# Kernel optimization log

Measured on AMD Instinct MI355X. Metric: run time of the kernel, lower is better.

The kernel has to match this reference:

```python
import jax, jax.numpy as jnp
import numpy as np

HEADS, FOLD_W, FOLD_H, PW, PH = 4, 2, 2, 2, 2


def setup_inputs() -> dict:
    key = jax.random.key(0)
    ks = jax.random.split(key, 4)
    B, C, W0, H0 = 64, 128, 56, 56
    hd = HEADS * 24  # 96
    return {
        "x": jax.random.normal(ks[0], (B, C, W0, H0), jnp.float32),
        "Wc": jax.random.normal(ks[1], (hd, C), jnp.float32) * 0.05,
        "bc": jnp.zeros((hd,), jnp.float32),
        "Wp": jax.random.normal(ks[2], (hd, C), jnp.float32) * 0.05,
        "bp": jnp.zeros((hd,), jnp.float32),
        "sim_alpha": jnp.ones((1,), jnp.float32),
        "sim_beta": jnp.zeros((1,), jnp.float32),
        "Wo": jax.random.normal(ks[3], (C, hd), jnp.float32) * 0.05,
        "bo": jnp.zeros((C,), jnp.float32),
    }


def _conv1x1(t, W, b):
    return jnp.einsum('oc,bcwh->bowh', W, t) + b[None, :, None, None]


def _forward(x, Wc, bc, Wp, bp, sim_alpha, sim_beta, Wo, bo):
    B, C, W0, H0 = x.shape
    value = _conv1x1(x, Wp, bp)   # [B, e*c, W0, H0]
    q = _conv1x1(x, Wc, bc)
    hd = q.shape[1] // HEADS
    # 'b (e c) w h -> (b e) c w h'
    split = lambda t: t.reshape(B * HEADS, hd, W0, H0)
    value, q = split(value), split(q)
    # fold: 'b c (f1 w) (f2 h) -> (b f1 f2) c w h'
    w2, h2 = W0 // FOLD_W, H0 // FOLD_H
    def fold(t):
        b0 = t.shape[0]
        return (t.reshape(b0, hd, FOLD_W, w2, FOLD_H, h2)
                 .transpose(0, 2, 4, 1, 3, 5)
                 .reshape(b0 * FOLD_W * FOLD_H, hd, w2, h2))
    value, q = fold(value), fold(q)
    b, c, w, h = q.shape
    # adaptive avg pool to (PW, PH): mean over equal blocks
    def adpool(t):
        return t.reshape(b, c, PW, w // PW, PH, h // PH).mean(axis=(3, 5))
    centers = adpool(q).reshape(b, c, PW * PH).transpose(0, 2, 1)          # [b, M, c]
    value_centers = adpool(value).reshape(b, c, PW * PH).transpose(0, 2, 1)
    qf = q.reshape(b, c, w * h).transpose(0, 2, 1)                          # [b, N, c]
    vf = value.reshape(b, c, w * h).transpose(0, 2, 1)
    eps = 1e-12
    cn = centers / jnp.clip(jnp.linalg.norm(centers, axis=-1, keepdims=True), eps)
    xn = qf / jnp.clip(jnp.linalg.norm(qf, axis=-1, keepdims=True), eps)
    sim = jax.nn.sigmoid(sim_beta + sim_alpha * jnp.einsum('bmc,bnc->bmn', cn, xn))  # [b, M, N]
    # hard top-1 assignment over centers axis
    idx = jnp.argmax(sim, axis=1)                                           # [b, N]
    mask = (jnp.arange(sim.shape[1])[None, :, None] == idx[:, None, :])
    sim = sim * mask
    # weighted combine (segment-sum over patches) instead of huge broadcast
    cluster = (jnp.einsum('bmn,bnc->bmc', sim, vf) + value_centers) / (sim.sum(-1, keepdims=True) + 1.0)
    patches = jnp.einsum('bmn,bmc->bnc', sim, cluster)                      # [b, N, c]
    patches = patches.transpose(0, 2, 1).reshape(b, c, w, h)
    # unfold: '(b f1 f2) c w h -> b c (f1 w) (f2 h)'
    patches = (patches.reshape(B * HEADS, FOLD_W, FOLD_H, c, w, h)
                      .transpose(0, 3, 1, 4, 2, 5)
                      .reshape(B * HEADS, c, W0, H0))
    patches = patches.reshape(B, HEADS * c, W0, H0)
    return _conv1x1(patches, Wo, bo)


def reference(x, Wc, bc, Wp, bp, sim_alpha, sim_beta, Wo, bo):
    return _forward(x, Wc, bc, Wp, bp, sim_alpha, sim_beta, Wo, bo)
```

## Files before the change

kernel.cpp:

```cpp
#include <hip/hip_runtime.h>
#include <math.h>

#define CIN 128
#define HD  96
#define SP  3136
#define ROW 56
#define SLAB 1568
#define YSTRIDE 9216

__global__ __launch_bounds__(256) void wtq_k(
    const float* __restrict__ Wc, float* __restrict__ Wt)
{
  const int idx = blockIdx.x * 256 + threadIdx.x;
  if (idx >= 96 * 128) return;
  const int o = idx >> 7, c = idx & 127;
  Wt[c * 96 + o] = Wc[idx];
}

__global__ __launch_bounds__(256) void pe_k(
    const float* __restrict__ Wo, const float* __restrict__ Wp,
    const float* __restrict__ bp, float* __restrict__ P, float* __restrict__ obp)
{
  const int e = blockIdx.x;
  __shared__ float ws[24][128];
  const int tid = threadIdx.x;
  for (int i = tid; i < 24 * 128; i += 256)
    ws[i >> 7][i & 127] = Wp[(size_t)(e * 24 + (i >> 7)) * CIN + (i & 127)];
  __syncthreads();
  const int co = tid & 127;
  const int cig = tid >> 7;
  float wo_r[24];
  #pragma unroll
  for (int c = 0; c < 24; ++c) wo_r[c] = Wo[(size_t)co * HD + e * 24 + c];
  for (int ci = cig * 64; ci < cig * 64 + 64; ++ci) {
    float s = 0.f;
    #pragma unroll
    for (int c = 0; c < 24; ++c) s = fmaf(wo_r[c], ws[c][ci], s);
    P[((size_t)e * 128 + ci) * 128 + co] = s;
  }
  if (cig == 0) {
    float s = 0.f;
    #pragma unroll
    for (int c = 0; c < 24; ++c) s = fmaf(wo_r[c], bp[e * 24 + c], s);
    obp[e * 128 + co] = s;
  }
}

__global__ __launch_bounds__(128) void q_conv(
    const float* __restrict__ x, const float* __restrict__ Wt,
    const float* __restrict__ bc, float* __restrict__ qbuf)
{
  const int st = blockIdx.x % 49;
  const int b  = blockIdx.x / 49;
  const float* xb = x + (size_t)b * CIN * SP + st * 64;

  __shared__ float xs[32][64];
  __shared__ float wl[32][96];

  const int tid = threadIdx.x;
  const int og = tid >> 4;
  const int sg = tid & 15;

  float acc[12][4];
  #pragma unroll
  for (int i = 0; i < 12; ++i) { acc[i][0]=0.f; acc[i][1]=0.f; acc[i][2]=0.f; acc[i][3]=0.f; }

  for (int kt = 0; kt < 4; ++kt) {
    __syncthreads();
    #pragma unroll
    for (int r = 0; r < 4; ++r) {
      const int i = tid + r * 128;
      const int cc = i >> 4, s4 = i & 15;
      float4 v = *reinterpret_cast<const float4*>(xb + (size_t)(kt*32 + cc) * SP + s4*4);
      *reinterpret_cast<float4*>(&xs[cc][s4*4]) = v;
    }
    #pragma unroll
    for (int r = 0; r < 6; ++r) {
      const int i = tid + r * 128;
      const int cl = i / 24, o4 = i % 24;
      float4 wv = *reinterpret_cast<const float4*>(Wt + (size_t)(kt*32 + cl) * 96 + o4*4);
      *reinterpret_cast<float4*>(&wl[cl][o4*4]) = wv;
    }
    __syncthreads();
    #pragma unroll
    for (int cc = 0; cc < 32; ++cc) {
      float xv[4];
      *reinterpret_cast<float4*>(xv) = *reinterpret_cast<const float4*>(&xs[cc][sg*4]);
      float wv[12];
      *reinterpret_cast<float4*>(wv + 0) = *reinterpret_cast<const float4*>(&wl[cc][og*12 + 0]);
      *reinterpret_cast<float4*>(wv + 4) = *reinterpret_cast<const float4*>(&wl[cc][og*12 + 4]);
      *reinterpret_cast<float4*>(wv + 8) = *reinterpret_cast<const float4*>(&wl[cc][og*12 + 8]);
      #pragma unroll
      for (int i = 0; i < 12; ++i)
        #pragma unroll
        for (int j = 0; j < 4; ++j)
          acc[i][j] = fmaf(wv[i], xv[j], acc[i][j]);
    }
  }
  #pragma unroll
  for (int i = 0; i < 12; ++i) {
    const int o = og * 12 + i;
    const float bias = bc[o];
    float4 v;
    v.x = acc[i][0] + bias; v.y = acc[i][1] + bias;
    v.z = acc[i][2] + bias; v.w = acc[i][3] + bias;
    *reinterpret_cast<float4*>(qbuf + ((size_t)b*96 + o) * SP + st*64 + sg*4) = v;
  }
}

__global__ __launch_bounds__(512, 4) void cluster_k(
    float* qbuf, const float* __restrict__ alpha_p, const float* __restrict__ beta_p)
{
  const int blk = blockIdx.x;
  const int f1  = blk & 1;
  const int be  = blk >> 1;
  const size_t base = (size_t)be * 24 * SP + (size_t)(f1 * 28) * ROW;
  float* qp = qbuf + base;

  __shared__ double cnd[24][8];
  __shared__ float  sbest[SLAB];
  __shared__ unsigned char ibest[SLAB];
  __shared__ float dnl[8];

  const int tid  = threadIdx.x;
  const int wid  = tid >> 6;
  const int lane = tid & 63;

  for (int c = wid; c < 24; c += 8) {
    const float* src = qp + (size_t)c * SP;
    double b0=0,b1=0,b2=0,b3=0,b4=0,b5=0,b6=0,b7=0;
    for (int n = lane; n < SLAB; n += 64) {
      const int w = n / 56, h = n - w * 56;
      const int hf = (h >= 28) ? (h - 28) : h;
      const int g  = ((h >= 28) ? 4 : 0) + ((w >= 14) ? 2 : 0) + ((hf >= 14) ? 1 : 0);
      const double val = (double)src[n];
      b0 += (g==0)?val:0.0; b1 += (g==1)?val:0.0;
      b2 += (g==2)?val:0.0; b3 += (g==3)?val:0.0;
      b4 += (g==4)?val:0.0; b5 += (g==5)?val:0.0;
      b6 += (g==6)?val:0.0; b7 += (g==7)?val:0.0;
    }
    #pragma unroll
    for (int m = 32; m >= 1; m >>= 1) {
      b0 += __shfl_xor(b0,m); b1 += __shfl_xor(b1,m);
      b2 += __shfl_xor(b2,m); b3 += __shfl_xor(b3,m);
      b4 += __shfl_xor(b4,m); b5 += __shfl_xor(b5,m);
      b6 += __shfl_xor(b6,m); b7 += __shfl_xor(b7,m);
    }
    if (lane == 0) {
      cnd[c][0]=b0*(1.0/196.0); cnd[c][1]=b1*(1.0/196.0);
      cnd[c][2]=b2*(1.0/196.0); cnd[c][3]=b3*(1.0/196.0);
      cnd[c][4]=b4*(1.0/196.0); cnd[c][5]=b5*(1.0/196.0);
      cnd[c][6]=b6*(1.0/196.0); cnd[c][7]=b7*(1.0/196.0);
    }
  }
  __syncthreads();
  if (tid < 8) {
    double s = 0.0;
    #pragma unroll
    for (int c = 0; c < 24; ++c) { double t = cnd[c][tid]; s += t * t; }
    const double inv = 1.0 / fmax(sqrt(s), 1e-12);
    #pragma unroll
    for (int c = 0; c < 24; ++c) cnd[c][tid] *= inv;
  }
  __syncthreads();

  const double alpha = (double)alpha_p[0];
  const double beta  = (double)beta_p[0];

  for (int n0 = tid; n0 < SLAB; n0 += 512) {
    const int h  = n0 % 56;
    const int gb = (h >= 28) ? 4 : 0;
    double z0=0,z1=0,z2=0,z3=0,nrm=0;
    for (int c = 0; c < 24; ++c) {
      const double qv = (double)qp[(size_t)c * SP + n0];
      z0 += cnd[c][gb+0]*qv; z1 += cnd[c][gb+1]*qv;
      z2 += cnd[c][gb+2]*qv; z3 += cnd[c][gb+3]*qv;
      nrm += qv*qv;
    }
    const double inv = 1.0 / fmax(sqrt(nrm), 1e-12);
    const double v0 = beta + alpha * (z0 * inv);
    const double v1 = beta + alpha * (z1 * inv);
    const double v2 = beta + alpha * (z2 * inv);
    const double v3 = beta + alpha * (z3 * inv);
    double zb = v0; int bi = 0;
    if (v1 > zb) { zb = v1; bi = 1; }
    if (v2 > zb) { zb = v2; bi = 2; }
    if (v3 > zb) { zb = v3; bi = 3; }
    sbest[n0] = (float)(1.0 / (1.0 + exp(-zb)));
    ibest[n0] = (unsigned char)(gb + bi);
  }
  __syncthreads();

  if (wid < 8) {
    float dn = 0.f;
    for (int ch = 0; ch < 25; ++ch) {
      const int n = ch * 64 + lane;
      const bool p = (n < SLAB) && (ibest[n] == (unsigned char)wid);
      dn += p ? sbest[n] : 0.f;
    }
    #pragma unroll
    for (int m = 32; m >= 1; m >>= 1) dn += __shfl_xor(dn, m);
    if (lane == 0) dnl[wid] = dn;
  }
  __syncthreads();

  for (int i = tid; i < SLAB; i += 512) {
    qp[i] = sbest[i];
    reinterpret_cast<unsigned int*>(qp + SP)[i] = (unsigned int)ibest[i];
  }
  if (tid < 8) qp[2 * (size_t)SP + tid] = dnl[tid];
}

__global__ __launch_bounds__(256, 2) void seg_k(
    float* qbuf, const float* __restrict__ x)
{
  const int bid = blockIdx.x;
  const int wh  = bid & 1;
  const int f2  = (bid >> 1) & 1;
  const int f1  = (bid >> 2) & 1;
  const int b   = bid >> 3;

  __shared__ float4 sq_l[392];
  __shared__ unsigned int gq_l[392];
  __shared__ float xT[56][130];
  __shared__ float ysum[16][128];
  __shared__ float xps[2][128];

  const int tid = threadIdx.x;
  const int c   = tid & 127;
  const int pg  = tid >> 7;

  for (int n = tid; n < 392; n += 256) {
    const int r = n / 28, hc = n - r * 28;
    const int n_slab = (wh * 14 + r) * 56 + f2 * 28 + hc;
    float4 s4; unsigned int gp = 0;
    #pragma unroll
    for (int e = 0; e < 4; ++e) {
      const float* qp = qbuf + (size_t)(b*4 + e) * 24 * SP + (size_t)(f1*28) * ROW;
      const float sv = qp[n_slab];
      const unsigned int gv = reinterpret_cast<const unsigned int*>(qp + SP)[n_slab];
      if (e==0) s4.x = sv; else if (e==1) s4.y = sv;
      else if (e==2) s4.z = sv; else s4.w = sv;
      gp |= (gv & 3u) << (2*e);
    }
    sq_l[n] = s4; gq_l[n] = gp;
  }

  float sa[16];
  #pragma unroll
  for (int i = 0; i < 16; ++i) sa[i] = 0.f;
  float xp0 = 0.f, xp1 = 0.f;

  const float* xb = x + (size_t)b * CIN * SP;
  const int rowbase = f1*28 + wh*14;

  for (int ch = 0; ch < 7; ++ch) {
    __syncthreads();
    #pragma unroll
    for (int k = 0; k < 7; ++k) {
      const int slot = tid + k * 256;
      const int c2 = slot / 14, p4 = slot - c2 * 14;
      const int rr = p4 / 7, col4 = p4 - rr * 7;
      const int w = rowbase + ch*2 + rr;
      const float4 v = *reinterpret_cast<const float4*>(
          xb + (size_t)c2 * SP + (size_t)w * ROW + f2*28 + col4*4);
      const int pxl = rr * 28 + col4 * 4;
      xT[pxl+0][c2] = v.x; xT[pxl+1][c2] = v.y;
      xT[pxl+2][c2] = v.z; xT[pxl+3][c2] = v.w;
    }
    __syncthreads();
    for (int i = 0; i < 28; ++i) {
      const int pxl = 2*i + pg;
      const int n   = ch*56 + pxl;
      const float4 s4 = sq_l[n];
      const int gp = __builtin_amdgcn_readfirstlane((int)gq_l[n]);
      const float xv = xT[pxl][c];
      {
        const int k = gp & 3;
        if      (k == 0) sa[0]  += s4.x * xv;
        else if (k == 1) sa[1]  += s4.x * xv;
        else if (k == 2) sa[2]  += s4.x * xv;
        else             sa[3]  += s4.x * xv;
      }
      {
        const int k = (gp >> 2) & 3;
        if      (k == 0) sa[4]  += s4.y * xv;
        else if (k == 1) sa[5]  += s4.y * xv;
        else if (k == 2) sa[6]  += s4.y * xv;
        else             sa[7]  += s4.y * xv;
      }
      {
        const int k = (gp >> 4) & 3;
        if      (k == 0) sa[8]  += s4.z * xv;
        else if (k == 1) sa[9]  += s4.z * xv;
        else if (k == 2) sa[10] += s4.z * xv;
        else             sa[11] += s4.z * xv;
      }
      {
        const int k = (gp >> 6) & 3;
        if      (k == 0) sa[12] += s4.w * xv;
        else if (k == 1) sa[13] += s4.w * xv;
        else if (k == 2) sa[14] += s4.w * xv;
        else             sa[15] += s4.w * xv;
      }
      const int hc = (pxl >= 28) ? (pxl - 28) : pxl;
      if (hc >= 14) xp1 += xv; else xp0 += xv;
    }
  }

  __syncthreads();
  if (pg == 0) {
    #pragma unroll
    for (int k = 0; k < 16; ++k) ysum[k][c] = sa[k];
    xps[0][c] = xp0; xps[1][c] = xp1;
  }
  __syncthreads();
  if (pg == 1) {
    #pragma unroll
    for (int k = 0; k < 16; ++k) ysum[k][c] += sa[k];
    xps[0][c] += xp0; xps[1][c] += xp1;
  }
  __syncthreads();

  float* ybase = qbuf + ((size_t)b*96 + 9) * SP + (size_t)f1 * YSTRIDE;
  for (int i = tid; i < 16*128; i += 256) {
    const int row = i >> 7, cc = i & 127;
    ybase[((wh*2 + f2)*16 + row)*128 + cc] = ysum[row][cc];
  }
  {
    const int hb = tid >> 7, cc = tid & 127;
    ybase[64*128 + (f2*4 + wh*2 + hb)*128 + cc] = xps[hb][cc];
  }
}

__global__ __launch_bounds__(256) void proj_k(
    float* qbuf, const float* __restrict__ P, const float* __restrict__ obp)
{
  const int bid = blockIdx.x;
  const int b = bid >> 1, f1 = bid & 1;
  __shared__ float ylds[32][128];
  __shared__ float invs[32];
  const int tid = threadIdx.x;

  if (tid < 32) {
    const int e = tid >> 3, g = tid & 7;
    const float* dnp = qbuf + ((size_t)(b*4 + e) * 24 + 2) * SP + (size_t)(f1*28) * ROW;
    invs[tid] = 1.f / (dnp[g] + 1.f);
  }
  __syncthreads();

  const float* yp = qbuf + ((size_t)b*96 + 9) * SP + (size_t)f1 * YSTRIDE;
  for (int i = tid; i < 32*128; i += 256) {
    const int eg = i >> 7, cc = i & 127;
    const int e = eg >> 3, g = eg & 7, ff2 = g >> 2, m = g & 3;
    const float v = yp[((0 + ff2)*16 + e*4 + m)*128 + cc]
                  + yp[((2 + ff2)*16 + e*4 + m)*128 + cc]
                  + yp[64*128 + g*128 + cc] * (1.f/196.f);
    ylds[eg][cc] = v * invs[eg];
  }
  __syncthreads();

  const int co = tid & 127;
  const int e0 = (tid >> 7) * 2;
  float a0[8], a1[8];
  const float o0 = obp[e0 * 128 + co], o1 = obp[(e0 + 1) * 128 + co];
  #pragma unroll
  for (int g = 0; g < 8; ++g) { a0[g] = o0; a1[g] = o1; }
  for (int ci = 0; ci < 128; ++ci) {
    const float p0 = P[((size_t)e0 * 128 + ci) * 128 + co];
    const float p1 = P[((size_t)(e0 + 1) * 128 + ci) * 128 + co];
    #pragma unroll
    for (int g = 0; g < 8; ++g) {
      a0[g] = fmaf(p0, ylds[e0 * 8 + g][ci], a0[g]);
      a1[g] = fmaf(p1, ylds[(e0 + 1) * 8 + g][ci], a1[g]);
    }
  }
  float* pout = qbuf + ((size_t)b * 96 + 3 + f1 * 3) * SP;
  #pragma unroll
  for (int g = 0; g < 8; ++g) {
    pout[(e0 * 8 + g) * 128 + co]       = a0[g];
    pout[((e0 + 1) * 8 + g) * 128 + co] = a1[g];
  }
}

__global__ __launch_bounds__(256) void out_k(
    const float* __restrict__ qbuf, const float* __restrict__ bo,
    float* __restrict__ out)
{
  const int bid = blockIdx.x;
  const int b   = bid / 28;
  const int rem = bid % 28;
  const int f1  = rem / 14;
  const int rp  = rem % 14;
  const int n0  = rp * 112;

  __shared__ float  proj_l[4096];
  __shared__ float4 s_l4[112];
  __shared__ unsigned int g_l[112];
  __shared__ float  out_l[56 * 132];

  const int tid = threadIdx.x;

  {
    const float4* pg = reinterpret_cast<const float4*>(
        qbuf + ((size_t)b * 96 + 3 + f1*3) * SP);
    float4* pl = reinterpret_cast<float4*>(proj_l);
    #pragma unroll
    for (int r = 0; r < 4; ++r) pl[tid + r * 256] = pg[tid + r * 256];
  }
  for (int i = tid; i < 112; i += 256) {
    float4 sv; unsigned int gp = 0;
    #pragma unroll
    for (int e = 0; e < 4; ++e) {
      const float* sp = qbuf + ((size_t)(b*4 + e) * 24) * SP + (size_t)(f1*28) * ROW;
      const float sval = sp[n0 + i];
      const unsigned int gv = reinterpret_cast<const unsigned int*>(sp + SP)[n0 + i];
      if (e == 0) sv.x = sval; else if (e == 1) sv.y = sval;
      else if (e == 2) sv.z = sval; else sv.w = sval;
      gp |= (gv & 7u) << (8 * e);
    }
    s_l4[i] = sv; g_l[i] = gp;
  }
  __syncthreads();

  const int cq  = tid & 31;
  const int sub = tid >> 5;
  const float4 bo4 = *reinterpret_cast<const float4*>(bo + cq * 4);
  const float4* pl4 = reinterpret_cast<const float4*>(proj_l);

  for (int chunk = 0; chunk < 2; ++chunk) {
    const int pbase = chunk * 56;
    #pragma unroll
    for (int i = 0; i < 7; ++i) {
      const int pxl = sub * 7 + i;
      const int px  = pbase + pxl;
      const float4 sv = s_l4[px];
      const unsigned int gp = g_l[px];
      float4 acc = bo4;
      {
        const float4 p = pl4[(0*8 + (gp        & 7u)) * 32 + cq];
        acc.x = fmaf(sv.x, p.x, acc.x); acc.y = fmaf(sv.x, p.y, acc.y);
        acc.z = fmaf(sv.x, p.z, acc.z); acc.w = fmaf(sv.x, p.w, acc.w);
      }
      {
        const float4 p = pl4[(1*8 + ((gp >> 8) & 7u)) * 32 + cq];
        acc.x = fmaf(sv.y, p.x, acc.x); acc.y = fmaf(sv.y, p.y, acc.y);
        acc.z = fmaf(sv.y, p.z, acc.z); acc.w = fmaf(sv.y, p.w, acc.w);
      }
      {
        const float4 p = pl4[(2*8 + ((gp >> 16) & 7u)) * 32 + cq];
        acc.x = fmaf(sv.z, p.x, acc.x); acc.y = fmaf(sv.z, p.y, acc.y);
        acc.z = fmaf(sv.z, p.z, acc.z); acc.w = fmaf(sv.z, p.w, acc.w);
      }
      {
        const float4 p = pl4[(3*8 + ((gp >> 24) & 7u)) * 32 + cq];
        acc.x = fmaf(sv.w, p.x, acc.x); acc.y = fmaf(sv.w, p.y, acc.y);
        acc.z = fmaf(sv.w, p.z, acc.z); acc.w = fmaf(sv.w, p.w, acc.w);
      }
      *reinterpret_cast<float4*>(&out_l[pxl * 132 + cq * 4]) = acc;
    }
    __syncthreads();
    for (int t = tid; t < 128 * 56; t += 256) {
      const int co = t / 56, pxl = t - co * 56;
      out[((size_t)b * 128 + co) * SP + (size_t)f1 * SLAB + n0 + pbase + pxl] =
          out_l[pxl * 132 + co];
    }
    __syncthreads();
  }
}

extern "C" void kernel_launch(void* const* d_in, const int* in_sizes, int n_in,
                              void* d_out, int out_size, void* d_ws, size_t ws_size,
                              hipStream_t stream) {
  const float* x  = (const float*)d_in[0];
  const float* Wc = (const float*)d_in[1];
  const float* bc = (const float*)d_in[2];
  const float* Wp = (const float*)d_in[3];
  const float* bp = (const float*)d_in[4];
  const float* sa = (const float*)d_in[5];
  const float* sb = (const float*)d_in[6];
  const float* Wo = (const float*)d_in[7];
  const float* bo = (const float*)d_in[8];
  float* out  = (float*)d_out;
  float* qbuf = (float*)d_ws;
  float* Pbuf = out;
  float* obpb = out + 65536;
  float* Wtq  = out + 66048;

  wtq_k    <<<dim3(48),      dim3(256), 0, stream>>>(Wc, Wtq);
  pe_k     <<<dim3(4),       dim3(256), 0, stream>>>(Wo, Wp, bp, Pbuf, obpb);
  q_conv   <<<dim3(64 * 49), dim3(128), 0, stream>>>(x, Wtq, bc, qbuf);
  cluster_k<<<dim3(512),     dim3(512), 0, stream>>>(qbuf, sa, sb);
  seg_k    <<<dim3(512),     dim3(256), 0, stream>>>(qbuf, x);
  proj_k   <<<dim3(128),     dim3(256), 0, stream>>>(qbuf, Pbuf, obpb);
  out_k    <<<dim3(1792),    dim3(256), 0, stream>>>(qbuf, bo, out);
}
```

Measured before the change: 233.0 us.

## Restructure q_conv to wave-uniform scalar weight loads with 512-thread blocks

The q projection kernel now uses 512 threads per block, eight waves each owning 12 output channels. Each lane handles one spatial position, and the weights are read straight from global memory at a wave-uniform address (via readfirstlane), so they can be fetched with scalar loads instead of staged through shared memory. This removes the weight LDS tile and one staging loop, and raises the number of waves per block. In exchange each thread does far fewer FMAs per x load (12 instead of 48), the outputs become scalar rather than float4 stores, and the x tile is reused less per thread.

```diff
diff --git a/kernel.cpp b/kernel.cpp
--- a/kernel.cpp
+++ b/kernel.cpp
@@ -46,7 +46,7 @@
   }
 }
 
-__global__ __launch_bounds__(128) void q_conv(
+__global__ __launch_bounds__(512) void q_conv(
     const float* __restrict__ x, const float* __restrict__ Wt,
     const float* __restrict__ bc, float* __restrict__ qbuf)
 {
@@ -55,56 +55,48 @@
   const float* xb = x + (size_t)b * CIN * SP + st * 64;
 
   __shared__ float xs[32][64];
-  __shared__ float wl[32][96];
-
-  const int tid = threadIdx.x;
-  const int og = tid >> 4;
-  const int sg = tid & 15;
-
-  float acc[12][4];
-  #pragma unroll
-  for (int i = 0; i < 12; ++i) { acc[i][0]=0.f; acc[i][1]=0.f; acc[i][2]=0.f; acc[i][3]=0.f; }
+
+  const int tid  = threadIdx.x;
+  const int lane = tid & 63;
+  const int o0   = __builtin_amdgcn_readfirstlane(tid >> 6) * 12;
+
+  float acc[12];
+  #pragma unroll
+  for (int i = 0; i < 12; ++i) acc[i] = 0.f;
 
   for (int kt = 0; kt < 4; ++kt) {
     __syncthreads();
-    #pragma unroll
-    for (int r = 0; r < 4; ++r) {
-      const int i = tid + r * 128;
-      const int cc = i >> 4, s4 = i & 15;
+    {
+      const int cc = tid >> 4, s4 = tid & 15;
       float4 v = *reinterpret_cast<const float4*>(xb + (size_t)(kt*32 + cc) * SP + s4*4);
       *reinterpret_cast<float4*>(&xs[cc][s4*4]) = v;
     }
-    #pragma unroll
-    for (int r = 0; r < 6; ++r) {
-      const int i = tid + r * 128;
-      const int cl = i / 24, o4 = i % 24;
-      float4 wv = *reinterpret_cast<const float4*>(Wt + (size_t)(kt*32 + cl) * 96 + o4*4);
-      *reinterpret_cast<float4*>(&wl[cl][o4*4]) = wv;
-    }
-    __syncthreads();
-    #pragma unroll
+    __syncthreads();
+    const float* wrow = Wt + (size_t)(kt * 32) * 96 + o0;
+    #pragma unroll 4
     for (int cc = 0; cc < 32; ++cc) {
-      float xv[4];
-      *reinterpret_cast<float4*>(xv) = *reinterpret_cast<const float4*>(&xs[cc][sg*4]);
-      float wv[12];
-      *reinterpret_cast<float4*>(wv + 0) = *reinterpret_cast<const float4*>(&wl[cc][og*12 + 0]);
-      *reinterpret_cast<float4*>(wv + 4) = *reinterpret_cast<const float4*>(&wl[cc][og*12 + 4]);
-      *reinterpret_cast<float4*>(wv + 8) = *reinterpret_cast<const float4*>(&wl[cc][og*12 + 8]);
-      #pragma unroll
-      for (int i = 0; i < 12; ++i)
-        #pragma unroll
-        for (int j = 0; j < 4; ++j)
-          acc[i][j] = fmaf(wv[i], xv[j], acc[i][j]);
+      const float xv = xs[cc][lane];
+      const float4 w0 = *reinterpret_cast<const float4*>(wrow + cc*96 + 0);
+      const float4 w1 = *reinterpret_cast<const float4*>(wrow + cc*96 + 4);
+      const float4 w2 = *reinterpret_cast<const float4*>(wrow + cc*96 + 8);
+      acc[0]  = fmaf(w0.x, xv, acc[0]);
+      acc[1]  = fmaf(w0.y, xv, acc[1]);
+      acc[2]  = fmaf(w0.z, xv, acc[2]);
+      acc[3]  = fmaf(w0.w, xv, acc[3]);
+      acc[4]  = fmaf(w1.x, xv, acc[4]);
+      acc[5]  = fmaf(w1.y, xv, acc[5]);
+      acc[6]  = fmaf(w1.z, xv, acc[6]);
+      acc[7]  = fmaf(w1.w, xv, acc[7]);
+      acc[8]  = fmaf(w2.x, xv, acc[8]);
+      acc[9]  = fmaf(w2.y, xv, acc[9]);
+      acc[10] = fmaf(w2.z, xv, acc[10]);
+      acc[11] = fmaf(w2.w, xv, acc[11]);
     }
   }
   #pragma unroll
   for (int i = 0; i < 12; ++i) {
-    const int o = og * 12 + i;
-    const float bias = bc[o];
-    float4 v;
-    v.x = acc[i][0] + bias; v.y = acc[i][1] + bias;
-    v.z = acc[i][2] + bias; v.w = acc[i][3] + bias;
-    *reinterpret_cast<float4*>(qbuf + ((size_t)b*96 + o) * SP + st*64 + sg*4) = v;
+    const int o = o0 + i;
+    qbuf[((size_t)b*96 + o) * SP + st*64 + lane] = acc[i] + bc[o];
   }
 }
 
@@ -489,7 +481,7 @@
 
   wtq_k    <<<dim3(48),      dim3(256), 0, stream>>>(Wc, Wtq);
   pe_k     <<<dim3(4),       dim3(256), 0, stream>>>(Wo, Wp, bp, Pbuf, obpb);
-  q_conv   <<<dim3(64 * 49), dim3(128), 0, stream>>>(x, Wtq, bc, qbuf);
+  q_conv   <<<dim3(64 * 49), dim3(512), 0, stream>>>(x, Wtq, bc, qbuf);
   cluster_k<<<dim3(512),     dim3(512), 0, stream>>>(qbuf, sa, sb);
   seg_k    <<<dim3(512),     dim3(256), 0, stream>>>(qbuf, x);
   proj_k   <<<dim3(128),     dim3(256), 0, stream>>>(qbuf, Pbuf, obpb);
```

Measured after the change: 226.2 us. -2.9%, faster.
